# Optimization experiments

Hardware: AMD Instinct MI355X
Metric: run time of the kernel (lower is better)

## Reference

```python
import jax, jax.numpy as jnp
import numpy as np


def setup_inputs() -> dict:
    key = jax.random.key(0)
    kq, kk, kv = jax.random.split(key, 3)
    B, S, H, D = 1, 4096, 16, 64
    q = jax.random.normal(kq, (B, S, H, D), dtype=jnp.float32)
    k = jax.random.normal(kk, (B, S, H, D), dtype=jnp.float32)
    v = jax.random.normal(kv, (B, S, H, D), dtype=jnp.float32)
    return {"q": q, "k": k, "v": v, "causal": 1}


def reference(q, k, v, causal):
    B, S, H, D = q.shape
    scale = D ** (-0.5)
    # scores: [B, H, S_q, S_k]
    scores = jnp.einsum("bqhd,bkhd->bhqk", q, k) * scale
    if causal:
        mask = jnp.triu(jnp.ones((S, S), dtype=bool), k=1)  # True above diagonal
        scores = jnp.where(mask, -jnp.inf, scores)
    attn = jax.nn.softmax(scores, axis=-1)
    out = jnp.einsum("bhqk,bkhd->bqhd", attn, v)
    return out
```

## Files before the change

### kernel.cpp

```cpp
#include <hip/hip_runtime.h>
#include <stdint.h>

#define S_LEN 4096
#define NH    16
#define HD    64
#define RSTR  (NH * HD)
#define LRSTR 18

typedef __attribute__((ext_vector_type(8))) __bf16 bf16x8;
typedef __attribute__((ext_vector_type(4))) short short4v;
typedef __attribute__((ext_vector_type(4))) float floatx4;

union BF8 { unsigned short u[8]; unsigned d[4]; uint4 q; bf16x8 v; };
union BF4 { unsigned short u[4]; unsigned d[2]; short4v s; };

__device__ __forceinline__ unsigned pkbf(float a, float b) {
    unsigned ua = __builtin_bit_cast(unsigned, a) + 0x8000u;
    unsigned ub = __builtin_bit_cast(unsigned, b) + 0x8000u;
    return __builtin_amdgcn_perm(ub, ua, 0x07060302u);
}

__device__ __forceinline__ floatx4 mfma16(short4v a, short4v b, floatx4 c) {
#if __has_builtin(__builtin_amdgcn_mfma_f32_16x16x16bf16_1k)
    return __builtin_amdgcn_mfma_f32_16x16x16bf16_1k(a, b, c, 0, 0, 0);
#else
    floatx4 d;
    asm volatile("v_mfma_f32_16x16x16_bf16 %0, %1, %2, %3\n\ts_nop 7\n\ts_nop 7"
                 : "=v"(d) : "v"(a), "v"(b), "v"(c));
    return d;
#endif
}

__device__ __forceinline__ void gl16(const void* g, void* l) {
#if __has_builtin(__builtin_amdgcn_global_load_lds)
    __builtin_amdgcn_global_load_lds((const __attribute__((address_space(1))) unsigned int*)g,
                                     (__attribute__((address_space(3))) unsigned int*)l, 16, 0, 0);
#else
    *(uint4*)l = *(const uint4*)g;
#endif
}

__global__ __launch_bounds__(256)
void pp_kv(const float* __restrict__ K, const float* __restrict__ V,
           unsigned short* __restrict__ Kz, unsigned short* __restrict__ Vz) {
    const int bid = blockIdx.x;
    const int h   = bid & 15;
    const int tau = bid >> 4;
    const int tid = threadIdx.x;
    {
        const int r = tid >> 2, gg = tid & 3;
        const float* kp = K + ((size_t)(64 * tau + r) * NH + h) * HD + 16 * gg;
        const float4 a = *reinterpret_cast<const float4*>(kp);
        const float4 b = *reinterpret_cast<const float4*>(kp + 4);
        const float4 c = *reinterpret_cast<const float4*>(kp + 8);
        const float4 d = *reinterpret_cast<const float4*>(kp + 12);
        uint4 f0, f1;
        f0.x = pkbf(a.x, a.y); f0.y = pkbf(a.z, a.w);
        f0.z = pkbf(b.x, b.y); f0.w = pkbf(b.z, b.w);
        f1.x = pkbf(c.x, c.y); f1.y = pkbf(c.z, c.w);
        f1.z = pkbf(d.x, d.y); f1.w = pkbf(d.z, d.w);
        unsigned short* out = Kz + ((size_t)(h * 64 + tau)) * 4096 + r * 64;
        *reinterpret_cast<uint4*>(out + (((2 * gg)     ^ (r & 7)) * 8)) = f0;
        *reinterpret_cast<uint4*>(out + (((2 * gg + 1) ^ (r & 7)) * 8)) = f1;
    }
    {
        const int dr = tid & 63, kg = tid >> 6;
        const float* vp = V + ((size_t)(64 * tau + 16 * kg) * NH + h) * HD + dr;
        float x[16];
        #pragma unroll
        for (int j = 0; j < 16; ++j) x[j] = vp[(size_t)j * RSTR];
        uint4 g0, g1;
        g0.x = pkbf(x[0],  x[1]);  g0.y = pkbf(x[2],  x[3]);
        g0.z = pkbf(x[4],  x[5]);  g0.w = pkbf(x[6],  x[7]);
        g1.x = pkbf(x[8],  x[9]);  g1.y = pkbf(x[10], x[11]);
        g1.z = pkbf(x[12], x[13]); g1.w = pkbf(x[14], x[15]);
        unsigned short* out = Vz + ((size_t)(h * 64 + tau)) * 4096 + dr * 64;
        *reinterpret_cast<uint4*>(out + (((2 * kg)     ^ (dr & 7)) * 8)) = g0;
        *reinterpret_cast<uint4*>(out + (((2 * kg + 1) ^ (dr & 7)) * 8)) = g1;
    }
}

__global__ __launch_bounds__(256, 3)
void fa_main(const float* __restrict__ Q, const unsigned short* __restrict__ Kz,
             const unsigned short* __restrict__ Vz, const int* __restrict__ causal_p,
             float* __restrict__ O) {
    __shared__ __align__(16) unsigned char smem[40960];
    unsigned short* Klds = (unsigned short*)smem;
    unsigned short* Vlds = (unsigned short*)(smem + 16384);
    unsigned short* Qlds = (unsigned short*)(smem + 32768);
    float* Lsum = (float*)smem;
    float* Lred = (float*)(smem + 16384);

    const int bid = blockIdx.x;
    const int h   = bid & 15;
    const int x   = 63 - (bid >> 4);
    const int q0  = x * 64;

    const int tid = threadIdx.x;
    const int wv  = tid >> 6;
    const int ln  = tid & 63;
    const int c16 = ln & 15;
    const int qd  = ln >> 4;
    const int causal = causal_p[0];

    const float SC = 0.18033688011112042f;

    {
        const int r = tid >> 2, gg = tid & 3;
        const float* qp = Q + ((size_t)(q0 + r) * NH + h) * HD + 16 * gg;
        const float4 a = *reinterpret_cast<const float4*>(qp);
        const float4 b = *reinterpret_cast<const float4*>(qp + 4);
        const float4 c = *reinterpret_cast<const float4*>(qp + 8);
        const float4 d = *reinterpret_cast<const float4*>(qp + 12);
        uint4 f0, f1;
        f0.x = pkbf(a.x * SC, a.y * SC); f0.y = pkbf(a.z * SC, a.w * SC);
        f0.z = pkbf(b.x * SC, b.y * SC); f0.w = pkbf(b.z * SC, b.w * SC);
        f1.x = pkbf(c.x * SC, c.y * SC); f1.y = pkbf(c.z * SC, c.w * SC);
        f1.z = pkbf(d.x * SC, d.y * SC); f1.w = pkbf(d.z * SC, d.w * SC);
        unsigned short* out = Qlds + r * 64;
        *reinterpret_cast<uint4*>(out + (((2 * gg)     ^ (r & 7)) * 8)) = f0;
        *reinterpret_cast<uint4*>(out + (((2 * gg + 1) ^ (r & 7)) * 8)) = f1;
    }

    const char* kg = (const char*)Kz + (size_t)h * 64 * 8192 + wv * 2048 + ln * 16;
    const char* vg = (const char*)Vz + (size_t)h * 64 * 8192 + wv * 2048 + ln * 16;
    char* kl = (char*)smem + wv * 2048 + ln * 16;
    char* vl = (char*)smem + 16384 + wv * 2048 + ln * 16;

#define GLDS_TILE(IT, BUF) do {                                  \
    const char* ks_ = kg + (size_t)(IT) * 8192;                  \
    const char* vs_ = vg + (size_t)(IT) * 8192;                  \
    char* kd_ = kl + (BUF) * 8192;                               \
    char* vd_ = vl + (BUF) * 8192;                               \
    gl16(ks_, kd_); gl16(ks_ + 1024, kd_ + 1024);                \
    gl16(vs_, vd_); gl16(vs_ + 1024, vd_ + 1024);                \
} while (0)

    const int nIter = causal ? (x + 1) : (S_LEN / 64);

    floatx4 acc[4][4];
    #pragma unroll
    for (int m = 0; m < 4; ++m)
        #pragma unroll
        for (int t = 0; t < 4; ++t) acc[m][t] = floatx4{0.f, 0.f, 0.f, 0.f};
    float lacc[4] = {0.f, 0.f, 0.f, 0.f};

    const int e7 = c16 & 7;
    const int o0 = (qd ^ e7) * 8;
    const int o1 = ((4 + qd) ^ e7) * 8;
    const int vo = ((2 * wv + (qd >> 1)) ^ e7) * 8 + (qd & 1) * 4;
    const int mlhs = 16 * wv + 4 * qd;

    GLDS_TILE(0, 0);
    __syncthreads();

    bf16x8 qh0[4], qh1[4];
    #pragma unroll
    for (int t = 0; t < 4; ++t) {
        const unsigned short* qrow = Qlds + (16 * t + c16) * 64;
        qh0[t] = *reinterpret_cast<const bf16x8*>(qrow + o0);
        qh1[t] = *reinterpret_cast<const bf16x8*>(qrow + o1);
    }

    int cur = 0;
    for (int it = 0; it < nIter; ++it) {
        if (it + 1 < nIter) GLDS_TILE(it + 1, cur ^ 1);

        const unsigned short* Kb = Klds + cur * 4096;
        const unsigned short* Vb = Vlds + cur * 4096;

        const unsigned short* krow = Kb + (16 * wv + c16) * 64;
        const bf16x8 kf0 = *reinterpret_cast<const bf16x8*>(krow + o0);
        const bf16x8 kf1 = *reinterpret_cast<const bf16x8*>(krow + o1);

        const bool maskit = (causal != 0) && (it == nIter - 1);

        BF4 pf[4];
        #pragma unroll
        for (int t = 0; t < 4; ++t) {
            floatx4 st = __builtin_amdgcn_mfma_f32_16x16x32_bf16(
                kf0, qh0[t], floatx4{0.f, 0.f, 0.f, 0.f}, 0, 0, 0);
            st = __builtin_amdgcn_mfma_f32_16x16x32_bf16(kf1, qh1[t], st, 0, 0, 0);
            float p[4];
            #pragma unroll
            for (int i = 0; i < 4; ++i) {
                float sv = st[i];
                if (maskit && (mlhs + i > 16 * t + c16)) sv = -1e30f;
                p[i] = __builtin_amdgcn_exp2f(sv);
            }
            lacc[t] += (p[0] + p[1]) + (p[2] + p[3]);
            pf[t].d[0] = pkbf(p[0], p[1]);
            pf[t].d[1] = pkbf(p[2], p[3]);
        }

        #pragma unroll
        for (int md = 0; md < 4; ++md) {
            BF4 vf;
            const unsigned short* vrow = Vb + (16 * md + c16) * 64 + vo;
            *reinterpret_cast<uint2*>(&vf.d[0]) = *reinterpret_cast<const uint2*>(vrow);
            #pragma unroll
            for (int t = 0; t < 4; ++t)
                acc[md][t] = mfma16(vf.s, pf[t].s, acc[md][t]);
        }

        __syncthreads();
        cur ^= 1;
    }

    #pragma unroll
    for (int t = 0; t < 4; ++t) {
        float lt = lacc[t];
        lt += __shfl_xor(lt, 16);
        lt += __shfl_xor(lt, 32);
        if (qd == 0) Lsum[wv * 64 + t * 16 + c16] = lt;
    }

    const int qi  = tid & 63;
    const int dg  = tid >> 6;
    const int lnr = 16 * dg + (qi & 15);
    const int jb  = 4 * (qi >> 4);
    float* orow = O + ((size_t)(q0 + qi) * NH + h) * HD;
    float inv = 0.f;

    for (int md = 0; md < 4; ++md) {
        float* Lw = Lred + (wv * 64 + ln) * LRSTR;
        #pragma unroll
        for (int t = 0; t < 4; ++t) {
            float2 w0; w0.x = acc[md][t][0]; w0.y = acc[md][t][1];
            float2 w1; w1.x = acc[md][t][2]; w1.y = acc[md][t][3];
            *reinterpret_cast<float2*>(&Lw[4 * t])     = w0;
            *reinterpret_cast<float2*>(&Lw[4 * t + 2]) = w1;
        }
        __syncthreads();
        if (md == 0) {
            const float l = Lsum[qi] + Lsum[64 + qi] + Lsum[128 + qi] + Lsum[192 + qi];
            inv = 1.0f / l;
        }
        float s0 = 0.f, s1 = 0.f, s2 = 0.f, s3 = 0.f;
        #pragma unroll
        for (int w = 0; w < 4; ++w) {
            const float* Lr = Lred + (w * 64 + lnr) * LRSTR + jb;
            s0 += Lr[0]; s1 += Lr[1]; s2 += Lr[2]; s3 += Lr[3];
        }
        floatx4 o; o[0] = s0 * inv; o[1] = s1 * inv; o[2] = s2 * inv; o[3] = s3 * inv;
        *reinterpret_cast<floatx4*>(orow + 16 * md + 4 * dg) = o;
        __syncthreads();
    }
}

extern "C" void kernel_launch(void* const* d_in, const int* in_sizes, int n_in,
                              void* d_out, int out_size, void* d_ws, size_t ws_size,
                              hipStream_t stream) {
    const float* q = (const float*)d_in[0];
    const float* k = (const float*)d_in[1];
    const float* v = (const float*)d_in[2];
    const int* causal = (const int*)d_in[3];
    float* out = (float*)d_out;
    unsigned short* Kz = (unsigned short*)d_ws;
    unsigned short* Vz = Kz + (size_t)NH * 64 * 4096;
    pp_kv<<<dim3(64 * NH), dim3(256), 0, stream>>>(k, v, Kz, Vz);
    fa_main<<<dim3(64 * NH), dim3(256), 0, stream>>>(q, Kz, Vz, causal, out);
}
```

Measured before the change: 146.3 us.

## Split attention waves 2x2 over query and key, shrink LDS, transpose V via LDS

The main kernel now splits its four waves into a 2x2 grid over query halves and key halves instead of having every wave cover all queries against a quarter of the keys. This halves the accumulator registers and cuts the cross-wave output reduction to a single pairwise combine through LDS. Q staging is moved to overlap the K buffer, with an extra barrier after the Q fragments are read, so LDS drops to 32KB and launch bounds allow 4 blocks per CU. The preprocessing kernel now transposes V through a shared tile with coalesced float4 loads instead of strided scalar global reads. In exchange, each wave loads twice as many K fragments per tile.

```diff
diff --git a/kernel.cpp b/kernel.cpp
--- a/kernel.cpp
+++ b/kernel.cpp
@@ -5,13 +5,11 @@
 #define NH    16
 #define HD    64
 #define RSTR  (NH * HD)
-#define LRSTR 18
 
 typedef __attribute__((ext_vector_type(8))) __bf16 bf16x8;
 typedef __attribute__((ext_vector_type(4))) short short4v;
 typedef __attribute__((ext_vector_type(4))) float floatx4;
 
-union BF8 { unsigned short u[8]; unsigned d[4]; uint4 q; bf16x8 v; };
 union BF4 { unsigned short u[4]; unsigned d[2]; short4v s; };
 
 __device__ __forceinline__ unsigned pkbf(float a, float b) {
@@ -43,6 +41,7 @@
 __global__ __launch_bounds__(256)
 void pp_kv(const float* __restrict__ K, const float* __restrict__ V,
            unsigned short* __restrict__ Kz, unsigned short* __restrict__ Vz) {
+    __shared__ __align__(16) float vt[64][68];
     const int bid = blockIdx.x;
     const int h   = bid & 15;
     const int tau = bid >> 4;
@@ -64,11 +63,19 @@
         *reinterpret_cast<uint4*>(out + (((2 * gg + 1) ^ (r & 7)) * 8)) = f1;
     }
     {
+        const int r = tid >> 2, ch = tid & 3;
+        const float* vrow = V + ((size_t)(64 * tau + r) * NH + h) * HD + 4 * ch;
+        #pragma unroll
+        for (int k2 = 0; k2 < 4; ++k2)
+            *reinterpret_cast<float4*>(&vt[r][4 * ch + 16 * k2]) =
+                *reinterpret_cast<const float4*>(vrow + 16 * k2);
+    }
+    __syncthreads();
+    {
         const int dr = tid & 63, kg = tid >> 6;
-        const float* vp = V + ((size_t)(64 * tau + 16 * kg) * NH + h) * HD + dr;
         float x[16];
         #pragma unroll
-        for (int j = 0; j < 16; ++j) x[j] = vp[(size_t)j * RSTR];
+        for (int j = 0; j < 16; ++j) x[j] = vt[16 * kg + j][dr];
         uint4 g0, g1;
         g0.x = pkbf(x[0],  x[1]);  g0.y = pkbf(x[2],  x[3]);
         g0.z = pkbf(x[4],  x[5]);  g0.w = pkbf(x[6],  x[7]);
@@ -80,16 +87,16 @@
     }
 }
 
-__global__ __launch_bounds__(256, 3)
+__global__ __launch_bounds__(256, 4)
 void fa_main(const float* __restrict__ Q, const unsigned short* __restrict__ Kz,
              const unsigned short* __restrict__ Vz, const int* __restrict__ causal_p,
              float* __restrict__ O) {
-    __shared__ __align__(16) unsigned char smem[40960];
+    __shared__ __align__(16) unsigned char smem[32768];
     unsigned short* Klds = (unsigned short*)smem;
     unsigned short* Vlds = (unsigned short*)(smem + 16384);
-    unsigned short* Qlds = (unsigned short*)(smem + 32768);
-    float* Lsum = (float*)smem;
-    float* Lred = (float*)(smem + 16384);
+    unsigned short* Qlds = (unsigned short*)(smem + 8192);
+    float* Lred = (float*)smem;
+    float* Lsum = (float*)(smem + 18432);
 
     const int bid = blockIdx.x;
     const int h   = bid & 15;
@@ -98,6 +105,8 @@
 
     const int tid = threadIdx.x;
     const int wv  = tid >> 6;
+    const int wq  = wv & 1;
+    const int wk  = wv >> 1;
     const int ln  = tid & 63;
     const int c16 = ln & 15;
     const int qd  = ln >> 4;
@@ -138,29 +147,30 @@
 
     const int nIter = causal ? (x + 1) : (S_LEN / 64);
 
-    floatx4 acc[4][4];
+    floatx4 acc[4][2];
     #pragma unroll
     for (int m = 0; m < 4; ++m)
         #pragma unroll
-        for (int t = 0; t < 4; ++t) acc[m][t] = floatx4{0.f, 0.f, 0.f, 0.f};
-    float lacc[4] = {0.f, 0.f, 0.f, 0.f};
+        for (int t = 0; t < 2; ++t) acc[m][t] = floatx4{0.f, 0.f, 0.f, 0.f};
+    float lacc[2] = {0.f, 0.f};
 
     const int e7 = c16 & 7;
     const int o0 = (qd ^ e7) * 8;
     const int o1 = ((4 + qd) ^ e7) * 8;
-    const int vo = ((2 * wv + (qd >> 1)) ^ e7) * 8 + (qd & 1) * 4;
-    const int mlhs = 16 * wv + 4 * qd;
+    const int vo0 = ((4 * wk + 0 + (qd >> 1)) ^ e7) * 8 + (qd & 1) * 4;
+    const int vo1 = ((4 * wk + 2 + (qd >> 1)) ^ e7) * 8 + (qd & 1) * 4;
 
     GLDS_TILE(0, 0);
     __syncthreads();
 
-    bf16x8 qh0[4], qh1[4];
+    bf16x8 qh0[2], qh1[2];
     #pragma unroll
-    for (int t = 0; t < 4; ++t) {
-        const unsigned short* qrow = Qlds + (16 * t + c16) * 64;
+    for (int t = 0; t < 2; ++t) {
+        const unsigned short* qrow = Qlds + (16 * (2 * wq + t) + c16) * 64;
         qh0[t] = *reinterpret_cast<const bf16x8*>(qrow + o0);
         qh1[t] = *reinterpret_cast<const bf16x8*>(qrow + o1);
     }
+    __syncthreads();
 
     int cur = 0;
     for (int it = 0; it < nIter; ++it) {
@@ -169,38 +179,50 @@
         const unsigned short* Kb = Klds + cur * 4096;
         const unsigned short* Vb = Vlds + cur * 4096;
 
-        const unsigned short* krow = Kb + (16 * wv + c16) * 64;
-        const bf16x8 kf0 = *reinterpret_cast<const bf16x8*>(krow + o0);
-        const bf16x8 kf1 = *reinterpret_cast<const bf16x8*>(krow + o1);
+        bf16x8 kf0[2], kf1[2];
+        #pragma unroll
+        for (int ks = 0; ks < 2; ++ks) {
+            const unsigned short* krow = Kb + (32 * wk + 16 * ks + c16) * 64;
+            kf0[ks] = *reinterpret_cast<const bf16x8*>(krow + o0);
+            kf1[ks] = *reinterpret_cast<const bf16x8*>(krow + o1);
+        }
 
         const bool maskit = (causal != 0) && (it == nIter - 1);
 
-        BF4 pf[4];
-        #pragma unroll
-        for (int t = 0; t < 4; ++t) {
-            floatx4 st = __builtin_amdgcn_mfma_f32_16x16x32_bf16(
-                kf0, qh0[t], floatx4{0.f, 0.f, 0.f, 0.f}, 0, 0, 0);
-            st = __builtin_amdgcn_mfma_f32_16x16x32_bf16(kf1, qh1[t], st, 0, 0, 0);
-            float p[4];
-            #pragma unroll
-            for (int i = 0; i < 4; ++i) {
-                float sv = st[i];
-                if (maskit && (mlhs + i > 16 * t + c16)) sv = -1e30f;
-                p[i] = __builtin_amdgcn_exp2f(sv);
+        BF4 pf[2][2];
+        #pragma unroll
+        for (int ks = 0; ks < 2; ++ks) {
+            const int kvb = 32 * wk + 16 * ks + 4 * qd;
+            #pragma unroll
+            for (int t = 0; t < 2; ++t) {
+                floatx4 st = __builtin_amdgcn_mfma_f32_16x16x32_bf16(
+                    kf0[ks], qh0[t], floatx4{0.f, 0.f, 0.f, 0.f}, 0, 0, 0);
+                st = __builtin_amdgcn_mfma_f32_16x16x32_bf16(kf1[ks], qh1[t], st, 0, 0, 0);
+                const int qloc = 16 * (2 * wq + t) + c16;
+                float p[4];
+                #pragma unroll
+                for (int i = 0; i < 4; ++i) {
+                    float sv = st[i];
+                    if (maskit && (kvb + i > qloc)) sv = -1e30f;
+                    p[i] = __builtin_amdgcn_exp2f(sv);
+                }
+                lacc[t] += (p[0] + p[1]) + (p[2] + p[3]);
+                pf[ks][t].d[0] = pkbf(p[0], p[1]);
+                pf[ks][t].d[1] = pkbf(p[2], p[3]);
             }
-            lacc[t] += (p[0] + p[1]) + (p[2] + p[3]);
-            pf[t].d[0] = pkbf(p[0], p[1]);
-            pf[t].d[1] = pkbf(p[2], p[3]);
         }
 
         #pragma unroll
         for (int md = 0; md < 4; ++md) {
-            BF4 vf;
-            const unsigned short* vrow = Vb + (16 * md + c16) * 64 + vo;
-            *reinterpret_cast<uint2*>(&vf.d[0]) = *reinterpret_cast<const uint2*>(vrow);
-            #pragma unroll
-            for (int t = 0; t < 4; ++t)
-                acc[md][t] = mfma16(vf.s, pf[t].s, acc[md][t]);
+            const unsigned short* vrow = Vb + (16 * md + c16) * 64;
+            BF4 vf0, vf1;
+            *reinterpret_cast<uint2*>(&vf0.d[0]) = *reinterpret_cast<const uint2*>(vrow + vo0);
+            *reinterpret_cast<uint2*>(&vf1.d[0]) = *reinterpret_cast<const uint2*>(vrow + vo1);
+            #pragma unroll
+            for (int t = 0; t < 2; ++t) {
+                acc[md][t] = mfma16(vf0.s, pf[0][t].s, acc[md][t]);
+                acc[md][t] = mfma16(vf1.s, pf[1][t].s, acc[md][t]);
+            }
         }
 
         __syncthreads();
@@ -208,43 +230,43 @@
     }
 
     #pragma unroll
-    for (int t = 0; t < 4; ++t) {
+    for (int t = 0; t < 2; ++t) {
         float lt = lacc[t];
         lt += __shfl_xor(lt, 16);
         lt += __shfl_xor(lt, 32);
-        if (qd == 0) Lsum[wv * 64 + t * 16 + c16] = lt;
-    }
-
-    const int qi  = tid & 63;
-    const int dg  = tid >> 6;
-    const int lnr = 16 * dg + (qi & 15);
-    const int jb  = 4 * (qi >> 4);
-    float* orow = O + ((size_t)(q0 + qi) * NH + h) * HD;
-    float inv = 0.f;
-
-    for (int md = 0; md < 4; ++md) {
-        float* Lw = Lred + (wv * 64 + ln) * LRSTR;
-        #pragma unroll
-        for (int t = 0; t < 4; ++t) {
-            float2 w0; w0.x = acc[md][t][0]; w0.y = acc[md][t][1];
-            float2 w1; w1.x = acc[md][t][2]; w1.y = acc[md][t][3];
-            *reinterpret_cast<float2*>(&Lw[4 * t])     = w0;
-            *reinterpret_cast<float2*>(&Lw[4 * t + 2]) = w1;
-        }
-        __syncthreads();
-        if (md == 0) {
-            const float l = Lsum[qi] + Lsum[64 + qi] + Lsum[128 + qi] + Lsum[192 + qi];
-            inv = 1.0f / l;
-        }
-        float s0 = 0.f, s1 = 0.f, s2 = 0.f, s3 = 0.f;
-        #pragma unroll
-        for (int w = 0; w < 4; ++w) {
-            const float* Lr = Lred + (w * 64 + lnr) * LRSTR + jb;
-            s0 += Lr[0]; s1 += Lr[1]; s2 += Lr[2]; s3 += Lr[3];
-        }
-        floatx4 o; o[0] = s0 * inv; o[1] = s1 * inv; o[2] = s2 * inv; o[3] = s3 * inv;
-        *reinterpret_cast<floatx4*>(orow + 16 * md + 4 * dg) = o;
-        __syncthreads();
+        if (qd == 0) Lsum[wk * 64 + wq * 32 + t * 16 + c16] = lt;
+    }
+    if (wk == 0) {
+        float* Lw = Lred + (wq * 64 + ln) * 36;
+        #pragma unroll
+        for (int md = 0; md < 4; ++md)
+            #pragma unroll
+            for (int t = 0; t < 2; ++t)
+                *reinterpret_cast<floatx4*>(&Lw[(md * 2 + t) * 4]) = acc[md][t];
+    }
+    __syncthreads();
+    if (wk == 1) {
+        const float* Lr = Lred + (wq * 64 + ln) * 36;
+        float inv[2];
+        #pragma unroll
+        for (int t = 0; t < 2; ++t) {
+            const int qidx = wq * 32 + t * 16 + c16;
+            inv[t] = 1.0f / (Lsum[qidx] + Lsum[64 + qidx]);
+        }
+        #pragma unroll
+        for (int md = 0; md < 4; ++md)
+            #pragma unroll
+            for (int t = 0; t < 2; ++t) {
+                const floatx4 b = *reinterpret_cast<const floatx4*>(&Lr[(md * 2 + t) * 4]);
+                const floatx4 a = acc[md][t];
+                floatx4 o;
+                o[0] = (a[0] + b[0]) * inv[t];
+                o[1] = (a[1] + b[1]) * inv[t];
+                o[2] = (a[2] + b[2]) * inv[t];
+                o[3] = (a[3] + b[3]) * inv[t];
+                const int q = q0 + 16 * (2 * wq + t) + c16;
+                *reinterpret_cast<floatx4*>(O + ((size_t)q * NH + h) * HD + 16 * md + 4 * qd) = o;
+            }
     }
 }
 
```

Result: no change. 148.4 us (+1.4%).

## Triple-buffer K/V tiles with depth-2 prefetch and stage V transpose through LDS

Applied to the files above, without the earlier changes.

The attention loop moves from double to triple buffering. It prefetches two K/V tiles ahead and waits on vmcnt before a single barrier per iteration, replacing the trailing __syncthreads, so global-to-LDS loads overlap more compute. The first two tiles are issued before the Q conversion, and Q now sits in the third K buffer slot. In the K/V preprocessing kernel, V rows are loaded coalesced into a padded LDS tile and then read transposed, instead of strided scalar global reads. LDS per block grows to 48KB, which may limit occupancy.

```diff
diff --git a/kernel.cpp b/kernel.cpp
--- a/kernel.cpp
+++ b/kernel.cpp
@@ -11,7 +11,6 @@
 typedef __attribute__((ext_vector_type(4))) short short4v;
 typedef __attribute__((ext_vector_type(4))) float floatx4;
 
-union BF8 { unsigned short u[8]; unsigned d[4]; uint4 q; bf16x8 v; };
 union BF4 { unsigned short u[4]; unsigned d[2]; short4v s; };
 
 __device__ __forceinline__ unsigned pkbf(float a, float b) {
@@ -43,6 +42,7 @@
 __global__ __launch_bounds__(256)
 void pp_kv(const float* __restrict__ K, const float* __restrict__ V,
            unsigned short* __restrict__ Kz, unsigned short* __restrict__ Vz) {
+    __shared__ __align__(16) float vt[64][68];
     const int bid = blockIdx.x;
     const int h   = bid & 15;
     const int tau = bid >> 4;
@@ -64,11 +64,19 @@
         *reinterpret_cast<uint4*>(out + (((2 * gg + 1) ^ (r & 7)) * 8)) = f1;
     }
     {
+        const int r = tid >> 2, ch = tid & 3;
+        const float* vrow = V + ((size_t)(64 * tau + r) * NH + h) * HD + 4 * ch;
+        #pragma unroll
+        for (int k2 = 0; k2 < 4; ++k2)
+            *reinterpret_cast<float4*>(&vt[r][4 * ch + 16 * k2]) =
+                *reinterpret_cast<const float4*>(vrow + 16 * k2);
+    }
+    __syncthreads();
+    {
         const int dr = tid & 63, kg = tid >> 6;
-        const float* vp = V + ((size_t)(64 * tau + 16 * kg) * NH + h) * HD + dr;
         float x[16];
         #pragma unroll
-        for (int j = 0; j < 16; ++j) x[j] = vp[(size_t)j * RSTR];
+        for (int j = 0; j < 16; ++j) x[j] = vt[16 * kg + j][dr];
         uint4 g0, g1;
         g0.x = pkbf(x[0],  x[1]);  g0.y = pkbf(x[2],  x[3]);
         g0.z = pkbf(x[4],  x[5]);  g0.w = pkbf(x[6],  x[7]);
@@ -84,10 +92,10 @@
 void fa_main(const float* __restrict__ Q, const unsigned short* __restrict__ Kz,
              const unsigned short* __restrict__ Vz, const int* __restrict__ causal_p,
              float* __restrict__ O) {
-    __shared__ __align__(16) unsigned char smem[40960];
+    __shared__ __align__(16) unsigned char smem[49152];
     unsigned short* Klds = (unsigned short*)smem;
-    unsigned short* Vlds = (unsigned short*)(smem + 16384);
-    unsigned short* Qlds = (unsigned short*)(smem + 32768);
+    unsigned short* Vlds = (unsigned short*)(smem + 24576);
+    unsigned short* Qlds = (unsigned short*)(smem + 16384);
     float* Lsum = (float*)smem;
     float* Lred = (float*)(smem + 16384);
 
@@ -104,6 +112,23 @@
     const int causal = causal_p[0];
 
     const float SC = 0.18033688011112042f;
+
+    const char* kg = (const char*)Kz + (size_t)h * 64 * 8192 + wv * 2048 + ln * 16;
+    const char* vg = (const char*)Vz + (size_t)h * 64 * 8192 + wv * 2048 + ln * 16;
+    char* kl = (char*)smem + wv * 2048 + ln * 16;
+    char* vl = (char*)smem + 24576 + wv * 2048 + ln * 16;
+
+#define GLDS_TILE(IT, BUF) do {                                  \
+    const char* ks_ = kg + (size_t)(IT) * 8192;                  \
+    const char* vs_ = vg + (size_t)(IT) * 8192;                  \
+    char* kd_ = kl + (BUF) * 8192;                               \
+    char* vd_ = vl + (BUF) * 8192;                               \
+    gl16(ks_, kd_); gl16(ks_ + 1024, kd_ + 1024);                \
+    gl16(vs_, vd_); gl16(vs_ + 1024, vd_ + 1024);                \
+} while (0)
+
+    GLDS_TILE(0, 0);
+    GLDS_TILE(1, 1);
 
     {
         const int r = tid >> 2, gg = tid & 3;
@@ -122,20 +147,6 @@
         *reinterpret_cast<uint4*>(out + (((2 * gg + 1) ^ (r & 7)) * 8)) = f1;
     }
 
-    const char* kg = (const char*)Kz + (size_t)h * 64 * 8192 + wv * 2048 + ln * 16;
-    const char* vg = (const char*)Vz + (size_t)h * 64 * 8192 + wv * 2048 + ln * 16;
-    char* kl = (char*)smem + wv * 2048 + ln * 16;
-    char* vl = (char*)smem + 16384 + wv * 2048 + ln * 16;
-
-#define GLDS_TILE(IT, BUF) do {                                  \
-    const char* ks_ = kg + (size_t)(IT) * 8192;                  \
-    const char* vs_ = vg + (size_t)(IT) * 8192;                  \
-    char* kd_ = kl + (BUF) * 8192;                               \
-    char* vd_ = vl + (BUF) * 8192;                               \
-    gl16(ks_, kd_); gl16(ks_ + 1024, kd_ + 1024);                \
-    gl16(vs_, vd_); gl16(vs_ + 1024, vd_ + 1024);                \
-} while (0)
-
     const int nIter = causal ? (x + 1) : (S_LEN / 64);
 
     floatx4 acc[4][4];
@@ -151,7 +162,6 @@
     const int vo = ((2 * wv + (qd >> 1)) ^ e7) * 8 + (qd & 1) * 4;
     const int mlhs = 16 * wv + 4 * qd;
 
-    GLDS_TILE(0, 0);
     __syncthreads();
 
     bf16x8 qh0[4], qh1[4];
@@ -161,13 +171,22 @@
         qh0[t] = *reinterpret_cast<const bf16x8*>(qrow + o0);
         qh1[t] = *reinterpret_cast<const bf16x8*>(qrow + o1);
     }
-
-    int cur = 0;
+    __syncthreads();
+
+    int br = 0;
+    int b2 = 2;
     for (int it = 0; it < nIter; ++it) {
-        if (it + 1 < nIter) GLDS_TILE(it + 1, cur ^ 1);
-
-        const unsigned short* Kb = Klds + cur * 4096;
-        const unsigned short* Vb = Vlds + cur * 4096;
+        if (it == nIter - 1) {
+            asm volatile("s_waitcnt vmcnt(0)" ::: "memory");
+        } else {
+            asm volatile("s_waitcnt vmcnt(4)" ::: "memory");
+        }
+        __builtin_amdgcn_s_barrier();
+
+        if (it + 2 < nIter) GLDS_TILE(it + 2, b2);
+
+        const unsigned short* Kb = Klds + br * 4096;
+        const unsigned short* Vb = Vlds + br * 4096;
 
         const unsigned short* krow = Kb + (16 * wv + c16) * 64;
         const bf16x8 kf0 = *reinterpret_cast<const bf16x8*>(krow + o0);
@@ -203,9 +222,11 @@
                 acc[md][t] = mfma16(vf.s, pf[t].s, acc[md][t]);
         }
 
-        __syncthreads();
-        cur ^= 1;
-    }
+        br = (br == 2) ? 0 : br + 1;
+        b2 = (b2 == 2) ? 0 : b2 + 1;
+    }
+
+    __syncthreads();
 
     #pragma unroll
     for (int t = 0; t < 4; ++t) {
```

After: 142.3 us. 2.7% less time.
